# Optimization experiments

Measured on AMD Instinct MI355X. Metric: run time of the kernel, lower is better.

Reference implementation:

```python
import jax, jax.numpy as jnp
import numpy as np

N_NODES = 100000
N_EDGES = 1600000
FACTOR = 0.5
REPEAT = 2


def setup_inputs() -> dict:
    key = jax.random.key(0)
    ks = jax.random.split(key, 8)
    x = jax.random.normal(ks[0], (N_NODES, 32), dtype=jnp.float32)
    edge_val = jax.random.uniform(ks[1], (N_EDGES,), dtype=jnp.float32)
    edge_row = jax.random.randint(ks[2], (N_EDGES,), 0, N_NODES)
    edge_col = jax.random.randint(ks[3], (N_EDGES,), 0, N_NODES)
    W1 = jax.random.normal(ks[4], (32, 64), dtype=jnp.float32) * 0.05
    b1 = jnp.zeros((64,), dtype=jnp.float32)
    W2 = jax.random.normal(ks[5], (64, 64), dtype=jnp.float32) * 0.05
    b2 = jnp.zeros((64,), dtype=jnp.float32)
    return {"x": x, "edge_val": edge_val, "edge_row": edge_row,
            "edge_col": edge_col, "W1": W1, "b1": b1, "W2": W2, "b2": b2}


def _spmm(edge_row, edge_col, edge_val, h):
    # out[r] += (factor * val_e) * h[c]  for each edge e=(r,c)
    gathered = (FACTOR * edge_val)[:, None] * h[edge_col]  # [E, D]
    return jax.ops.segment_sum(gathered, edge_row, num_segments=N_NODES)


def _propagate(edge_row, edge_col, edge_val, h):
    # h = (factor*A)^repeat @ h
    for _ in range(REPEAT):
        h = _spmm(edge_row, edge_col, edge_val, h)
    return h


def reference(x, edge_val, edge_row, edge_col, W1, b1, W2, b2):
    # layer 1: propagate -> linear -> relu
    h = _propagate(edge_row, edge_col, edge_val, x)
    h = jax.nn.relu(h @ W1 + b1)
    # layer 2: propagate -> linear -> identity
    h = _propagate(edge_row, edge_col, edge_val, h)
    h = h @ W2 + b2
    return h
```

## Files before the change

kernel.cpp:

```cpp
#include <hip/hip_runtime.h>
#include <hip/hip_bf16.h>


#define REGION_SHIFT 9
#define REGION_SIZE  (1 << REGION_SHIFT)
#define COL_MASK 0x1FFFF
#define GBUILD 256

typedef unsigned short u16;
typedef unsigned int   u32;
typedef __attribute__((ext_vector_type(8))) short bf16x8;
typedef __attribute__((ext_vector_type(4))) float f32x4;

__device__ inline float bflo(u32 w) { return __uint_as_float(w << 16); }
__device__ inline float bfhi(u32 w) { return __uint_as_float(w & 0xffff0000u); }
__device__ inline u32 bfpack(float a, float b) {
    u32 ua = __float_as_uint(a), ub = __float_as_uint(b);
    ua = (ua + 0x7fffu + ((ua >> 16) & 1u)) >> 16;
    ub = (ub + 0x7fffu + ((ub >> 16) & 1u)) & 0xffff0000u;
    return ua | ub;
}
__device__ inline u16 bf1(float f) {
    u32 u = __float_as_uint(f);
    return (u16)((u + 0x7fffu + ((u >> 16) & 1u)) >> 16);
}

__global__ void region_count_kernel(const int* __restrict__ er, int E,
                                    int* __restrict__ partial,
                                    const float* __restrict__ x,
                                    u16* __restrict__ xb, int n4,
                                    const float* __restrict__ W1,
                                    const float* __restrict__ W2,
                                    u16* __restrict__ W1f,
                                    u16* __restrict__ W2f) {
    for (int i = blockIdx.x * 256 + threadIdx.x; i < n4; i += gridDim.x * 256) {
        float4 a = reinterpret_cast<const float4*>(x)[i];
        uint2 o;
        o.x = bfpack(a.x, a.y);
        o.y = bfpack(a.z, a.w);
        reinterpret_cast<uint2*>(xb)[i] = o;
    }
    if (blockIdx.x == 0) {
        for (int idx = threadIdx.x; idx < 2048; idx += 256) {
            int j = idx & 7, n16 = (idx >> 3) & 15;
            int quad = (idx >> 7) & 3, t = (idx >> 9) & 3;
            W1f[idx] = bf1(W1[(quad * 8 + j) * 64 + t * 16 + n16]);
        }
        for (int idx = threadIdx.x; idx < 4096; idx += 256) {
            int j = idx & 7, n16 = (idx >> 3) & 15;
            int quad = (idx >> 7) & 3, half = (idx >> 9) & 1, t = (idx >> 10) & 3;
            W2f[idx] = bf1(W2[(half * 32 + quad * 8 + j) * 64 + t * 16 + n16]);
        }
    }
    __shared__ int hist[256];
    int t = threadIdx.x;
    hist[t] = 0;
    __syncthreads();
    int chunk = (E + gridDim.x - 1) / gridDim.x;
    int s = blockIdx.x * chunk;
    int e = min(E, s + chunk);
    for (int i = s + t; i < e; i += 256)
        atomicAdd(&hist[er[i] >> REGION_SHIFT], 1);
    __syncthreads();
    partial[blockIdx.x * 256 + t] = hist[t];
}

__global__ void region_scan_kernel(const int* __restrict__ partial,
                                   int* __restrict__ region_off,
                                   int nreg, int E, int G) {
    __shared__ int s[256];
    int t = threadIdx.x;
    int total = 0;
    if (t < nreg)
        for (int b = 0; b < G; b++) total += partial[b * 256 + t];
    s[t] = (t < nreg) ? total : 0;
    __syncthreads();
    for (int off = 1; off < 256; off <<= 1) {
        int x = (t >= off) ? s[t - off] : 0;
        __syncthreads();
        s[t] += x;
        __syncthreads();
    }
    if (t < nreg) region_off[t] = s[t] - total;
    if (t == 0) region_off[nreg] = E;
}

__global__ void region_base_kernel(int* __restrict__ partial,
                                   const int* __restrict__ region_off, int nreg) {
    __shared__ int s[256];
    int r = blockIdx.x;
    if (r >= nreg) return;
    int t = threadIdx.x;
    int c = partial[t * 256 + r];
    s[t] = c;
    __syncthreads();
    for (int off = 1; off < 256; off <<= 1) {
        int x = (t >= off) ? s[t - off] : 0;
        __syncthreads();
        s[t] += x;
        __syncthreads();
    }
    partial[t * 256 + r] = region_off[r] + s[t] - c;
}

__global__ void coarse_scatter_kernel(const int* __restrict__ er,
                                      const int* __restrict__ ec,
                                      const float* __restrict__ ev, int E,
                                      const int* __restrict__ partial,
                                      int2* __restrict__ stg) {
    __shared__ int cnt2[256], gbase[256];
    int t = threadIdx.x;
    cnt2[t] = 0;
    gbase[t] = partial[blockIdx.x * 256 + t];
    __syncthreads();
    int chunk = (E + gridDim.x - 1) / gridDim.x;
    int s0 = blockIdx.x * chunk;
    int e0 = min(E, s0 + chunk);
    for (int i = s0 + t; i < e0; i += 256) {
        int r = er[i];
        int b = r >> REGION_SHIFT;
        int rank = atomicAdd(&cnt2[b], 1);
        int2 rec;
        rec.x = ec[i] | ((r & (REGION_SIZE - 1)) << 17);
        rec.y = (int)bf1(0.5f * ev[i]);
        stg[gbase[b] + rank] = rec;
    }
}

__global__ void region_sort_kernel(const int2* __restrict__ stg,
                                   const int* __restrict__ region_off,
                                   int* __restrict__ row_ptr,
                                   u32* __restrict__ cv, int N, int E) {
    __shared__ int hist[REGION_SIZE];
    __shared__ int wp_local[REGION_SIZE];
    __shared__ int psum[256];
    int cb = blockIdx.x;
    int lo = cb << REGION_SHIFT;
    if (lo >= N) return;
    int hi = min(lo + REGION_SIZE, N);
    int cnt = hi - lo;
    int t = threadIdx.x;
    for (int r = t; r < cnt; r += 256) hist[r] = 0;
    __syncthreads();
    int start = region_off[cb];
    int end   = region_off[cb + 1];
    for (int q = start + t; q < end; q += 256)
        atomicAdd(&hist[stg[q].x >> 17], 1);
    __syncthreads();
    int a0 = (2 * t     < cnt) ? hist[2 * t]     : 0;
    int a1 = (2 * t + 1 < cnt) ? hist[2 * t + 1] : 0;
    psum[t] = a0 + a1;
    __syncthreads();
    for (int off = 1; off < 256; off <<= 1) {
        int x = (t >= off) ? psum[t - off] : 0;
        __syncthreads();
        psum[t] += x;
        __syncthreads();
    }
    int excl = psum[t] - (a0 + a1);
    if (2 * t < cnt) {
        wp_local[2 * t] = start + excl;
        row_ptr[lo + 2 * t] = start + excl;
    }
    if (2 * t + 1 < cnt) {
        wp_local[2 * t + 1] = start + excl + a0;
        row_ptr[lo + 2 * t + 1] = start + excl + a0;
    }
    if (cb == 0 && t == 0) row_ptr[N] = E;
    __syncthreads();
    for (int q = start + t; q < end; q += 256) {
        int2 e = stg[q];
        int lr = e.x >> 17;
        int p = atomicAdd(&wp_local[lr], 1);
        cv[p] = ((u32)e.y << 17) | ((u32)e.x & COL_MASK);
    }
}

__device__ inline void fma8(float acc[8], float v, uint4 w) {
    acc[0] = fmaf(v, bflo(w.x), acc[0]); acc[1] = fmaf(v, bfhi(w.x), acc[1]);
    acc[2] = fmaf(v, bflo(w.y), acc[2]); acc[3] = fmaf(v, bfhi(w.y), acc[3]);
    acc[4] = fmaf(v, bflo(w.z), acc[4]); acc[5] = fmaf(v, bfhi(w.z), acc[5]);
    acc[6] = fmaf(v, bflo(w.w), acc[6]); acc[7] = fmaf(v, bfhi(w.w), acc[7]);
}
__device__ inline float cvval(u32 q) { return __uint_as_float((q >> 17) << 16); }

template <int D>
__device__ inline void spmm_row(const u16* __restrict__ h,
                                const u32* __restrict__ cv,
                                int start, int end, int sub, float acc[8]) {
    int j = start;
    for (; j + 8 <= end; j += 8) {
        u32 q0 = cv[j],     q1 = cv[j + 1], q2 = cv[j + 2], q3 = cv[j + 3];
        u32 q4 = cv[j + 4], q5 = cv[j + 5], q6 = cv[j + 6], q7 = cv[j + 7];
        uint4 w0 = reinterpret_cast<const uint4*>(h + (size_t)(q0 & COL_MASK) * D)[sub];
        uint4 w1 = reinterpret_cast<const uint4*>(h + (size_t)(q1 & COL_MASK) * D)[sub];
        uint4 w2 = reinterpret_cast<const uint4*>(h + (size_t)(q2 & COL_MASK) * D)[sub];
        uint4 w3 = reinterpret_cast<const uint4*>(h + (size_t)(q3 & COL_MASK) * D)[sub];
        uint4 w4 = reinterpret_cast<const uint4*>(h + (size_t)(q4 & COL_MASK) * D)[sub];
        uint4 w5 = reinterpret_cast<const uint4*>(h + (size_t)(q5 & COL_MASK) * D)[sub];
        uint4 w6 = reinterpret_cast<const uint4*>(h + (size_t)(q6 & COL_MASK) * D)[sub];
        uint4 w7 = reinterpret_cast<const uint4*>(h + (size_t)(q7 & COL_MASK) * D)[sub];
        fma8(acc, cvval(q0), w0);
        fma8(acc, cvval(q1), w1);
        fma8(acc, cvval(q2), w2);
        fma8(acc, cvval(q3), w3);
        fma8(acc, cvval(q4), w4);
        fma8(acc, cvval(q5), w5);
        fma8(acc, cvval(q6), w6);
        fma8(acc, cvval(q7), w7);
    }
    for (; j + 4 <= end; j += 4) {
        u32 q0 = cv[j], q1 = cv[j + 1], q2 = cv[j + 2], q3 = cv[j + 3];
        uint4 w0 = reinterpret_cast<const uint4*>(h + (size_t)(q0 & COL_MASK) * D)[sub];
        uint4 w1 = reinterpret_cast<const uint4*>(h + (size_t)(q1 & COL_MASK) * D)[sub];
        uint4 w2 = reinterpret_cast<const uint4*>(h + (size_t)(q2 & COL_MASK) * D)[sub];
        uint4 w3 = reinterpret_cast<const uint4*>(h + (size_t)(q3 & COL_MASK) * D)[sub];
        fma8(acc, cvval(q0), w0);
        fma8(acc, cvval(q1), w1);
        fma8(acc, cvval(q2), w2);
        fma8(acc, cvval(q3), w3);
    }
    for (; j < end; j++) {
        u32 q = cv[j];
        uint4 w = reinterpret_cast<const uint4*>(h + (size_t)(q & COL_MASK) * D)[sub];
        fma8(acc, cvval(q), w);
    }
}

template <int D, bool FINAL>
__global__ __launch_bounds__(256) void spmm_bf16_kernel(
        const u16* __restrict__ h,
        const int* __restrict__ row_ptr,
        const u32* __restrict__ cv,
        void* __restrict__ outp,
        const float* __restrict__ bias,
        int N) {
    constexpr int LPR = D / 8;
    int gid = blockIdx.x * 256 + threadIdx.x;
    int row = gid / LPR;
    int sub = gid % LPR;
    if (row >= N) return;
    int start = row_ptr[row];
    int end   = row_ptr[row + 1];
    float acc[8] = {0.f, 0.f, 0.f, 0.f, 0.f, 0.f, 0.f, 0.f};
    spmm_row<D>(h, cv, start, end, sub, acc);
    if (FINAL) {
        float* op = (float*)outp + (size_t)row * 64 + sub * 8;
#pragma unroll
        for (int k = 0; k < 8; k++) acc[k] += bias[sub * 8 + k];
        reinterpret_cast<float4*>(op)[0] = make_float4(acc[0], acc[1], acc[2], acc[3]);
        reinterpret_cast<float4*>(op)[1] = make_float4(acc[4], acc[5], acc[6], acc[7]);
    } else {
        u16* ob = (u16*)outp + (size_t)row * D + sub * 8;
        uint4 o;
        o.x = bfpack(acc[0], acc[1]);
        o.y = bfpack(acc[2], acc[3]);
        o.z = bfpack(acc[4], acc[5]);
        o.w = bfpack(acc[6], acc[7]);
        reinterpret_cast<uint4*>(ob)[0] = o;
    }
}

__global__ __launch_bounds__(256) void spmm_dense_kernel(
        const u16* __restrict__ h,
        const int* __restrict__ row_ptr,
        const u32* __restrict__ cv,
        const u16* __restrict__ W1f,
        const float* __restrict__ b1,
        const u16* __restrict__ W2f,
        u16* __restrict__ outb,
        int N) {
    __shared__ __align__(16) u16 tiles[4][16][80];
    int tid = threadIdx.x;
    int lane = tid & 63;
    int wave = tid >> 6;
    int tilebase = blockIdx.x * 64 + wave * 16;
    if (tilebase >= N) return;
    int gid = blockIdx.x * 256 + tid;
    int row = gid >> 2;
    int sub = gid & 3;

    bool vr = row < N;
    int start = vr ? row_ptr[row] : 0;
    int end   = vr ? row_ptr[row + 1] : 0;
    float acc[8] = {0.f, 0.f, 0.f, 0.f, 0.f, 0.f, 0.f, 0.f};
    spmm_row<32>(h, cv, start, end, sub, acc);

    u16 (*tile)[80] = tiles[wave];
    {
        uint4 o;
        o.x = bfpack(acc[0], acc[1]);
        o.y = bfpack(acc[2], acc[3]);
        o.z = bfpack(acc[4], acc[5]);
        o.w = bfpack(acc[6], acc[7]);
        *reinterpret_cast<uint4*>(&tile[lane >> 2][sub * 8]) = o;
    }

    int n16 = lane & 15;
    int quad = lane >> 4;
    bf16x8 w1f[4];
    bf16x8 w2f[4][2];
#pragma unroll
    for (int t = 0; t < 4; t++) {
        w1f[t] = *reinterpret_cast<const bf16x8*>(&W1f[((t * 4 + quad) * 16 + n16) * 8]);
        w2f[t][0] = *reinterpret_cast<const bf16x8*>(&W2f[(((t * 2 + 0) * 4 + quad) * 16 + n16) * 8]);
        w2f[t][1] = *reinterpret_cast<const bf16x8*>(&W2f[(((t * 2 + 1) * 4 + quad) * 16 + n16) * 8]);
    }
    float b1v[4];
#pragma unroll
    for (int t = 0; t < 4; t++) b1v[t] = b1[t * 16 + n16];

    bf16x8 a1 = *reinterpret_cast<const bf16x8*>(&tile[n16][quad * 8]);
    f32x4 zero = {0.f, 0.f, 0.f, 0.f};
    f32x4 c[4];
#pragma unroll
    for (int t = 0; t < 4; t++)
        c[t] = __builtin_amdgcn_mfma_f32_16x16x32_bf16(a1, w1f[t], zero, 0, 0, 0);

#pragma unroll
    for (int t = 0; t < 4; t++)
#pragma unroll
        for (int i = 0; i < 4; i++)
            tile[quad * 4 + i][t * 16 + n16] = bf1(fmaxf(c[t][i] + b1v[t], 0.f));

    bf16x8 a2_0 = *reinterpret_cast<const bf16x8*>(&tile[n16][quad * 8]);
    bf16x8 a2_1 = *reinterpret_cast<const bf16x8*>(&tile[n16][32 + quad * 8]);
    f32x4 d[4];
#pragma unroll
    for (int t = 0; t < 4; t++) {
        d[t] = __builtin_amdgcn_mfma_f32_16x16x32_bf16(a2_0, w2f[t][0], zero, 0, 0, 0);
        d[t] = __builtin_amdgcn_mfma_f32_16x16x32_bf16(a2_1, w2f[t][1], d[t], 0, 0, 0);
    }

#pragma unroll
    for (int t = 0; t < 4; t++)
#pragma unroll
        for (int i = 0; i < 4; i++)
            tile[quad * 4 + i][t * 16 + n16] = bf1(d[t][i]);

#pragma unroll
    for (int half = 0; half < 2; half++) {
        int g = half * 512 + lane * 8;
        int r = g >> 6, cc = g & 63;
        int grow = tilebase + r;
        if (grow < N)
            *reinterpret_cast<uint4*>(outb + (size_t)grow * 64 + cc) =
                *reinterpret_cast<const uint4*>(&tile[r][cc]);
    }
}

extern "C" void kernel_launch(void* const* d_in, const int* in_sizes, int n_in,
                              void* d_out, int out_size, void* d_ws, size_t ws_size,
                              hipStream_t stream) {
    const float* x        = (const float*)d_in[0];
    const float* edge_val = (const float*)d_in[1];
    const int*   edge_row = (const int*)d_in[2];
    const int*   edge_col = (const int*)d_in[3];
    const float* W1       = (const float*)d_in[4];
    const float* b1       = (const float*)d_in[5];
    const float* W2       = (const float*)d_in[6];
    const float* b2       = (const float*)d_in[7];
    float* out = (float*)d_out;

    const int N = in_sizes[0] / 32;
    const int E = in_sizes[1];
    const int NREG = (N + REGION_SIZE - 1) >> REGION_SHIFT;

    u16* xb  = (u16*)d_out;
    u16* t0b = xb + (size_t)N * 32;
    u16* t2b = (u16*)d_out + (size_t)N * 64;

    u16*  t3b = (u16*)d_ws;
    int2* stg = (int2*)d_ws;
    int*  row_ptr    = (int*)((char*)d_ws + (size_t)N * 64 * 2);
    int*  region_off = row_ptr + (N + 1);
    int*  partial    = region_off + (NREG + 1);
    size_t wOff = (((size_t)((char*)(partial + GBUILD * 256) - (char*)d_ws)) + 15) & ~(size_t)15;
    u16* W1f = (u16*)((char*)d_ws + wOff);
    u16* W2f = W1f + 2048;
    size_t cvOff = (((size_t)((char*)(W2f + 4096) - (char*)d_ws)) + 15) & ~(size_t)15;
    u32* cv = (u32*)((char*)d_ws + cvOff);

    int n4 = (N * 32) / 4;

    region_count_kernel<<<GBUILD, 256, 0, stream>>>(edge_row, E, partial, x, xb, n4,
                                                    W1, W2, W1f, W2f);
    region_scan_kernel<<<1, 256, 0, stream>>>(partial, region_off, NREG, E, GBUILD);
    region_base_kernel<<<NREG, 256, 0, stream>>>(partial, region_off, NREG);
    coarse_scatter_kernel<<<GBUILD, 256, 0, stream>>>(edge_row, edge_col, edge_val,
                                                      E, partial, stg);
    region_sort_kernel<<<NREG, 256, 0, stream>>>(stg, region_off, row_ptr, cv, N, E);

    int g32 = (N * 4 + 255) / 256;
    int g64 = (N * 8 + 255) / 256;

    spmm_bf16_kernel<32, false><<<g32, 256, 0, stream>>>(xb, row_ptr, cv, t0b, nullptr, N);
    spmm_dense_kernel<<<g32, 256, 0, stream>>>(t0b, row_ptr, cv, W1f, b1, W2f, t2b, N);
    spmm_bf16_kernel<64, false><<<g64, 256, 0, stream>>>(t2b, row_ptr, cv, t3b, nullptr, N);
    spmm_bf16_kernel<64, true><<<g64, 256, 0, stream>>>(t3b, row_ptr, cv, out, b2, N);
}
```

Baseline: 284.2 us.

## Fuse CSR build kernels into one persistent kernel with grid barriers

Merges the five graph-preprocessing kernels (region count, scan, base offsets, coarse scatter, region sort) into a single 256-block kernel that separates the phases with a software grid barrier built on global atomics. This is meant to remove four kernel launch gaps and their tail effects. It adds a memset for the barrier counter. It relies on all 256 blocks being co-resident, and the barrier spin and fences cost time at each phase.

```diff
diff --git a/kernel.cpp b/kernel.cpp
--- a/kernel.cpp
+++ b/kernel.cpp
@@ -5,7 +5,7 @@
 #define REGION_SHIFT 9
 #define REGION_SIZE  (1 << REGION_SHIFT)
 #define COL_MASK 0x1FFFF
-#define GBUILD 256
+#define NBLK 256
 
 typedef unsigned short u16;
 typedef unsigned int   u32;
@@ -25,154 +25,152 @@
     return (u16)((u + 0x7fffu + ((u >> 16) & 1u)) >> 16);
 }
 
-__global__ void region_count_kernel(const int* __restrict__ er, int E,
-                                    int* __restrict__ partial,
-                                    const float* __restrict__ x,
-                                    u16* __restrict__ xb, int n4,
-                                    const float* __restrict__ W1,
-                                    const float* __restrict__ W2,
-                                    u16* __restrict__ W1f,
-                                    u16* __restrict__ W2f) {
-    for (int i = blockIdx.x * 256 + threadIdx.x; i < n4; i += gridDim.x * 256) {
+__device__ inline void gridbar(int* __restrict__ bar) {
+    __syncthreads();
+    if (threadIdx.x == 0) {
+        __threadfence();
+        int g = __hip_atomic_load(&bar[1], __ATOMIC_RELAXED, __HIP_MEMORY_SCOPE_AGENT);
+        int a = __hip_atomic_fetch_add(&bar[0], 1, __ATOMIC_ACQ_REL, __HIP_MEMORY_SCOPE_AGENT);
+        if (a == NBLK - 1) {
+            __hip_atomic_store(&bar[0], 0, __ATOMIC_RELAXED, __HIP_MEMORY_SCOPE_AGENT);
+            __hip_atomic_fetch_add(&bar[1], 1, __ATOMIC_ACQ_REL, __HIP_MEMORY_SCOPE_AGENT);
+        } else {
+            while (__hip_atomic_load(&bar[1], __ATOMIC_ACQUIRE, __HIP_MEMORY_SCOPE_AGENT) == g)
+                __builtin_amdgcn_s_sleep(8);
+        }
+        __threadfence();
+    }
+    __syncthreads();
+}
+
+__global__ __launch_bounds__(256) void build_fused_kernel(
+        const int* __restrict__ er, const int* __restrict__ ec,
+        const float* __restrict__ ev, int E,
+        const float* __restrict__ x, u16* __restrict__ xb, int n4,
+        const float* __restrict__ W1, const float* __restrict__ W2,
+        u16* __restrict__ W1f, u16* __restrict__ W2f,
+        int* __restrict__ partial, int* __restrict__ region_off,
+        int2* __restrict__ stg, int* __restrict__ row_ptr,
+        u32* __restrict__ cv, int N, int nreg, int* __restrict__ bar) {
+    __shared__ int sh_a[REGION_SIZE];
+    __shared__ int sh_b[REGION_SIZE];
+    __shared__ int sh_p[256];
+    int t  = threadIdx.x;
+    int cb = blockIdx.x;
+
+    for (int i = cb * 256 + t; i < n4; i += NBLK * 256) {
         float4 a = reinterpret_cast<const float4*>(x)[i];
         uint2 o;
         o.x = bfpack(a.x, a.y);
         o.y = bfpack(a.z, a.w);
         reinterpret_cast<uint2*>(xb)[i] = o;
     }
-    if (blockIdx.x == 0) {
-        for (int idx = threadIdx.x; idx < 2048; idx += 256) {
+    if (cb == 0) {
+        for (int idx = t; idx < 2048; idx += 256) {
             int j = idx & 7, n16 = (idx >> 3) & 15;
-            int quad = (idx >> 7) & 3, t = (idx >> 9) & 3;
-            W1f[idx] = bf1(W1[(quad * 8 + j) * 64 + t * 16 + n16]);
-        }
-        for (int idx = threadIdx.x; idx < 4096; idx += 256) {
+            int quad = (idx >> 7) & 3, tt = (idx >> 9) & 3;
+            W1f[idx] = bf1(W1[(quad * 8 + j) * 64 + tt * 16 + n16]);
+        }
+        for (int idx = t; idx < 4096; idx += 256) {
             int j = idx & 7, n16 = (idx >> 3) & 15;
-            int quad = (idx >> 7) & 3, half = (idx >> 9) & 1, t = (idx >> 10) & 3;
-            W2f[idx] = bf1(W2[(half * 32 + quad * 8 + j) * 64 + t * 16 + n16]);
-        }
-    }
-    __shared__ int hist[256];
-    int t = threadIdx.x;
-    hist[t] = 0;
-    __syncthreads();
-    int chunk = (E + gridDim.x - 1) / gridDim.x;
-    int s = blockIdx.x * chunk;
-    int e = min(E, s + chunk);
-    for (int i = s + t; i < e; i += 256)
-        atomicAdd(&hist[er[i] >> REGION_SHIFT], 1);
-    __syncthreads();
-    partial[blockIdx.x * 256 + t] = hist[t];
-}
-
-__global__ void region_scan_kernel(const int* __restrict__ partial,
-                                   int* __restrict__ region_off,
-                                   int nreg, int E, int G) {
-    __shared__ int s[256];
-    int t = threadIdx.x;
-    int total = 0;
-    if (t < nreg)
-        for (int b = 0; b < G; b++) total += partial[b * 256 + t];
-    s[t] = (t < nreg) ? total : 0;
-    __syncthreads();
-    for (int off = 1; off < 256; off <<= 1) {
-        int x = (t >= off) ? s[t - off] : 0;
-        __syncthreads();
-        s[t] += x;
-        __syncthreads();
-    }
-    if (t < nreg) region_off[t] = s[t] - total;
-    if (t == 0) region_off[nreg] = E;
-}
-
-__global__ void region_base_kernel(int* __restrict__ partial,
-                                   const int* __restrict__ region_off, int nreg) {
-    __shared__ int s[256];
-    int r = blockIdx.x;
-    if (r >= nreg) return;
-    int t = threadIdx.x;
-    int c = partial[t * 256 + r];
-    s[t] = c;
-    __syncthreads();
-    for (int off = 1; off < 256; off <<= 1) {
-        int x = (t >= off) ? s[t - off] : 0;
-        __syncthreads();
-        s[t] += x;
-        __syncthreads();
-    }
-    partial[t * 256 + r] = region_off[r] + s[t] - c;
-}
-
-__global__ void coarse_scatter_kernel(const int* __restrict__ er,
-                                      const int* __restrict__ ec,
-                                      const float* __restrict__ ev, int E,
-                                      const int* __restrict__ partial,
-                                      int2* __restrict__ stg) {
-    __shared__ int cnt2[256], gbase[256];
-    int t = threadIdx.x;
-    cnt2[t] = 0;
-    gbase[t] = partial[blockIdx.x * 256 + t];
-    __syncthreads();
-    int chunk = (E + gridDim.x - 1) / gridDim.x;
-    int s0 = blockIdx.x * chunk;
+            int quad = (idx >> 7) & 3, half = (idx >> 9) & 1, tt = (idx >> 10) & 3;
+            W2f[idx] = bf1(W2[(half * 32 + quad * 8 + j) * 64 + tt * 16 + n16]);
+        }
+    }
+    sh_a[t] = 0;
+    __syncthreads();
+    int chunk = (E + NBLK - 1) / NBLK;
+    int s0 = cb * chunk;
     int e0 = min(E, s0 + chunk);
+    for (int i = s0 + t; i < e0; i += 256)
+        atomicAdd(&sh_a[er[i] >> REGION_SHIFT], 1);
+    __syncthreads();
+    partial[cb * 256 + t] = sh_a[t];
+    gridbar(bar);
+
+    if (cb == 0) {
+        int total = 0;
+        if (t < nreg)
+            for (int b = 0; b < NBLK; b++) total += partial[b * 256 + t];
+        sh_p[t] = (t < nreg) ? total : 0;
+        __syncthreads();
+        for (int off = 1; off < 256; off <<= 1) {
+            int xv = (t >= off) ? sh_p[t - off] : 0;
+            __syncthreads();
+            sh_p[t] += xv;
+            __syncthreads();
+        }
+        if (t < nreg) region_off[t] = sh_p[t] - total;
+        if (t == 0) region_off[nreg] = E;
+    }
+    gridbar(bar);
+
+    if (cb < nreg) {
+        int c = partial[t * 256 + cb];
+        sh_p[t] = c;
+        __syncthreads();
+        for (int off = 1; off < 256; off <<= 1) {
+            int xv = (t >= off) ? sh_p[t - off] : 0;
+            __syncthreads();
+            sh_p[t] += xv;
+            __syncthreads();
+        }
+        partial[t * 256 + cb] = region_off[cb] + sh_p[t] - c;
+    }
+    gridbar(bar);
+
+    sh_a[t] = 0;
+    sh_b[t] = partial[cb * 256 + t];
+    __syncthreads();
     for (int i = s0 + t; i < e0; i += 256) {
         int r = er[i];
         int b = r >> REGION_SHIFT;
-        int rank = atomicAdd(&cnt2[b], 1);
+        int rank = atomicAdd(&sh_a[b], 1);
         int2 rec;
         rec.x = ec[i] | ((r & (REGION_SIZE - 1)) << 17);
         rec.y = (int)bf1(0.5f * ev[i]);
-        stg[gbase[b] + rank] = rec;
-    }
-}
-
-__global__ void region_sort_kernel(const int2* __restrict__ stg,
-                                   const int* __restrict__ region_off,
-                                   int* __restrict__ row_ptr,
-                                   u32* __restrict__ cv, int N, int E) {
-    __shared__ int hist[REGION_SIZE];
-    __shared__ int wp_local[REGION_SIZE];
-    __shared__ int psum[256];
-    int cb = blockIdx.x;
-    int lo = cb << REGION_SHIFT;
-    if (lo >= N) return;
-    int hi = min(lo + REGION_SIZE, N);
-    int cnt = hi - lo;
-    int t = threadIdx.x;
-    for (int r = t; r < cnt; r += 256) hist[r] = 0;
-    __syncthreads();
-    int start = region_off[cb];
-    int end   = region_off[cb + 1];
-    for (int q = start + t; q < end; q += 256)
-        atomicAdd(&hist[stg[q].x >> 17], 1);
-    __syncthreads();
-    int a0 = (2 * t     < cnt) ? hist[2 * t]     : 0;
-    int a1 = (2 * t + 1 < cnt) ? hist[2 * t + 1] : 0;
-    psum[t] = a0 + a1;
-    __syncthreads();
-    for (int off = 1; off < 256; off <<= 1) {
-        int x = (t >= off) ? psum[t - off] : 0;
-        __syncthreads();
-        psum[t] += x;
-        __syncthreads();
-    }
-    int excl = psum[t] - (a0 + a1);
-    if (2 * t < cnt) {
-        wp_local[2 * t] = start + excl;
-        row_ptr[lo + 2 * t] = start + excl;
-    }
-    if (2 * t + 1 < cnt) {
-        wp_local[2 * t + 1] = start + excl + a0;
-        row_ptr[lo + 2 * t + 1] = start + excl + a0;
-    }
-    if (cb == 0 && t == 0) row_ptr[N] = E;
-    __syncthreads();
-    for (int q = start + t; q < end; q += 256) {
-        int2 e = stg[q];
-        int lr = e.x >> 17;
-        int p = atomicAdd(&wp_local[lr], 1);
-        cv[p] = ((u32)e.y << 17) | ((u32)e.x & COL_MASK);
+        stg[sh_b[b] + rank] = rec;
+    }
+    gridbar(bar);
+
+    if (cb < nreg) {
+        int lo = cb << REGION_SHIFT;
+        int hi = min(lo + REGION_SIZE, N);
+        int cnt = hi - lo;
+        for (int r = t; r < cnt; r += 256) sh_a[r] = 0;
+        __syncthreads();
+        int start = region_off[cb];
+        int end   = region_off[cb + 1];
+        for (int q = start + t; q < end; q += 256)
+            atomicAdd(&sh_a[stg[q].x >> 17], 1);
+        __syncthreads();
+        int a0 = (2 * t     < cnt) ? sh_a[2 * t]     : 0;
+        int a1 = (2 * t + 1 < cnt) ? sh_a[2 * t + 1] : 0;
+        sh_p[t] = a0 + a1;
+        __syncthreads();
+        for (int off = 1; off < 256; off <<= 1) {
+            int xv = (t >= off) ? sh_p[t - off] : 0;
+            __syncthreads();
+            sh_p[t] += xv;
+            __syncthreads();
+        }
+        int excl = sh_p[t] - (a0 + a1);
+        if (2 * t < cnt) {
+            sh_b[2 * t] = start + excl;
+            row_ptr[lo + 2 * t] = start + excl;
+        }
+        if (2 * t + 1 < cnt) {
+            sh_b[2 * t + 1] = start + excl + a0;
+            row_ptr[lo + 2 * t + 1] = start + excl + a0;
+        }
+        if (cb == 0 && t == 0) row_ptr[N] = E;
+        __syncthreads();
+        for (int q = start + t; q < end; q += 256) {
+            int2 e = stg[q];
+            int lr = e.x >> 17;
+            int p = atomicAdd(&sh_b[lr], 1);
+            cv[p] = ((u32)e.y << 17) | ((u32)e.x & COL_MASK);
+        }
     }
 }
 
@@ -375,21 +373,20 @@
     int*  row_ptr    = (int*)((char*)d_ws + (size_t)N * 64 * 2);
     int*  region_off = row_ptr + (N + 1);
     int*  partial    = region_off + (NREG + 1);
-    size_t wOff = (((size_t)((char*)(partial + GBUILD * 256) - (char*)d_ws)) + 15) & ~(size_t)15;
+    size_t wOff = (((size_t)((char*)(partial + NBLK * 256) - (char*)d_ws)) + 15) & ~(size_t)15;
     u16* W1f = (u16*)((char*)d_ws + wOff);
     u16* W2f = W1f + 2048;
     size_t cvOff = (((size_t)((char*)(W2f + 4096) - (char*)d_ws)) + 15) & ~(size_t)15;
     u32* cv = (u32*)((char*)d_ws + cvOff);
+    size_t barOff = (cvOff + (size_t)E * 4 + 255) & ~(size_t)255;
+    int* bar = (int*)((char*)d_ws + barOff);
 
     int n4 = (N * 32) / 4;
 
-    region_count_kernel<<<GBUILD, 256, 0, stream>>>(edge_row, E, partial, x, xb, n4,
-                                                    W1, W2, W1f, W2f);
-    region_scan_kernel<<<1, 256, 0, stream>>>(partial, region_off, NREG, E, GBUILD);
-    region_base_kernel<<<NREG, 256, 0, stream>>>(partial, region_off, NREG);
-    coarse_scatter_kernel<<<GBUILD, 256, 0, stream>>>(edge_row, edge_col, edge_val,
-                                                      E, partial, stg);
-    region_sort_kernel<<<NREG, 256, 0, stream>>>(stg, region_off, row_ptr, cv, N, E);
+    hipMemsetAsync(bar, 0, 16, stream);
+    build_fused_kernel<<<NBLK, 256, 0, stream>>>(
+        edge_row, edge_col, edge_val, E, x, xb, n4,
+        W1, W2, W1f, W2f, partial, region_off, stg, row_ptr, cv, N, NREG, bar);
 
     int g32 = (N * 4 + 255) / 256;
     int g64 = (N * 8 + 255) / 256;
```

After: 450.5 us. 1.59x slower.

## Merge region scan kernels, split staging into key/value arrays, cache region in LDS

Applied to the files above, without the earlier changes.

Fuses the single-block region scan and per-region base kernels into one kernel, where each block recomputes its region offset by reducing the partial counts of earlier regions. The staging buffer changes from int2 records to separate u32 key and u16 value arrays, which cuts staging bytes. The region sort kernel loads each region's edges into LDS once and reuses them for both the histogram and scatter passes, falling back to global memory past the capacity. In exchange it uses much more LDS per block and does redundant prefix work in the scan.

```diff
diff --git a/kernel.cpp b/kernel.cpp
--- a/kernel.cpp
+++ b/kernel.cpp
@@ -6,6 +6,7 @@
 #define REGION_SIZE  (1 << REGION_SHIFT)
 #define COL_MASK 0x1FFFF
 #define GBUILD 256
+#define K4CAP 9216
 
 typedef unsigned short u16;
 typedef unsigned int   u32;
@@ -65,53 +66,51 @@
     partial[blockIdx.x * 256 + t] = hist[t];
 }
 
-__global__ void region_scan_kernel(const int* __restrict__ partial,
-                                   int* __restrict__ region_off,
-                                   int nreg, int E, int G) {
-    __shared__ int s[256];
-    int t = threadIdx.x;
-    int total = 0;
-    if (t < nreg)
-        for (int b = 0; b < G; b++) total += partial[b * 256 + t];
-    s[t] = (t < nreg) ? total : 0;
-    __syncthreads();
-    for (int off = 1; off < 256; off <<= 1) {
-        int x = (t >= off) ? s[t - off] : 0;
-        __syncthreads();
-        s[t] += x;
-        __syncthreads();
-    }
-    if (t < nreg) region_off[t] = s[t] - total;
-    if (t == 0) region_off[nreg] = E;
-}
-
-__global__ void region_base_kernel(int* __restrict__ partial,
-                                   const int* __restrict__ region_off, int nreg) {
+__global__ void region_scanbase_kernel(const int* __restrict__ partial,
+                                       int* __restrict__ bases,
+                                       int* __restrict__ region_off,
+                                       int nreg, int E, int G) {
     __shared__ int s[256];
     int r = blockIdx.x;
     if (r >= nreg) return;
     int t = threadIdx.x;
-    int c = partial[t * 256 + r];
+    int rowsum = 0;
+    const int* prow = partial + t * 256;
+    for (int q = 0; q < r; q++) rowsum += prow[q];
+    s[t] = rowsum;
+    __syncthreads();
+    for (int off = 128; off > 0; off >>= 1) {
+        if (t < off) s[t] += s[t + off];
+        __syncthreads();
+    }
+    int off_r = s[0];
+    __syncthreads();
+    if (t == 0) {
+        region_off[r] = off_r;
+        if (r == 0) region_off[nreg] = E;
+    }
+    int c = prow[r];
     s[t] = c;
     __syncthreads();
     for (int off = 1; off < 256; off <<= 1) {
-        int x = (t >= off) ? s[t - off] : 0;
+        int xv = (t >= off) ? s[t - off] : 0;
         __syncthreads();
-        s[t] += x;
+        s[t] += xv;
         __syncthreads();
     }
-    partial[t * 256 + r] = region_off[r] + s[t] - c;
+    bases[t * 256 + r] = off_r + s[t] - c;
 }
 
 __global__ void coarse_scatter_kernel(const int* __restrict__ er,
                                       const int* __restrict__ ec,
                                       const float* __restrict__ ev, int E,
-                                      const int* __restrict__ partial,
-                                      int2* __restrict__ stg) {
+                                      const int* __restrict__ bases,
+                                      u32* __restrict__ stgk,
+                                      u16* __restrict__ stgv) {
     __shared__ int cnt2[256], gbase[256];
     int t = threadIdx.x;
     cnt2[t] = 0;
-    gbase[t] = partial[blockIdx.x * 256 + t];
+    gbase[t] = bases[blockIdx.x * 256 + t];
     __syncthreads();
     int chunk = (E + gridDim.x - 1) / gridDim.x;
     int s0 = blockIdx.x * chunk;
@@ -120,17 +119,19 @@
         int r = er[i];
         int b = r >> REGION_SHIFT;
         int rank = atomicAdd(&cnt2[b], 1);
-        int2 rec;
-        rec.x = ec[i] | ((r & (REGION_SIZE - 1)) << 17);
-        rec.y = (int)bf1(0.5f * ev[i]);
-        stg[gbase[b] + rank] = rec;
-    }
-}
-
-__global__ void region_sort_kernel(const int2* __restrict__ stg,
+        int p = gbase[b] + rank;
+        stgk[p] = (u32)ec[i] | ((u32)(r & (REGION_SIZE - 1)) << 17);
+        stgv[p] = bf1(0.5f * ev[i]);
+    }
+}
+
+__global__ void region_sort_kernel(const u32* __restrict__ stgk,
+                                   const u16* __restrict__ stgv,
                                    const int* __restrict__ region_off,
                                    int* __restrict__ row_ptr,
                                    u32* __restrict__ cv, int N, int E) {
+    __shared__ u32 sk[K4CAP];
+    __shared__ u16 sv[K4CAP];
     __shared__ int hist[REGION_SIZE];
     __shared__ int wp_local[REGION_SIZE];
     __shared__ int psum[256];
@@ -141,11 +142,18 @@
     int cnt = hi - lo;
     int t = threadIdx.x;
     for (int r = t; r < cnt; r += 256) hist[r] = 0;
-    __syncthreads();
     int start = region_off[cb];
     int end   = region_off[cb + 1];
-    for (int q = start + t; q < end; q += 256)
-        atomicAdd(&hist[stg[q].x >> 17], 1);
+    for (int q = start + t; q < end; q += 256) {
+        int idx = q - start;
+        if (idx < K4CAP) { sk[idx] = stgk[q]; sv[idx] = stgv[q]; }
+    }
+    __syncthreads();
+    for (int q = start + t; q < end; q += 256) {
+        int idx = q - start;
+        u32 key = (idx < K4CAP) ? sk[idx] : stgk[q];
+        atomicAdd(&hist[key >> 17], 1);
+    }
     __syncthreads();
     int a0 = (2 * t     < cnt) ? hist[2 * t]     : 0;
     int a1 = (2 * t + 1 < cnt) ? hist[2 * t + 1] : 0;
@@ -169,10 +177,13 @@
     if (cb == 0 && t == 0) row_ptr[N] = E;
     __syncthreads();
     for (int q = start + t; q < end; q += 256) {
-        int2 e = stg[q];
-        int lr = e.x >> 17;
+        int idx = q - start;
+        u32 key; u32 val;
+        if (idx < K4CAP) { key = sk[idx]; val = sv[idx]; }
+        else             { key = stgk[q]; val = stgv[q]; }
+        int lr = key >> 17;
         int p = atomicAdd(&wp_local[lr], 1);
-        cv[p] = ((u32)e.y << 17) | ((u32)e.x & COL_MASK);
+        cv[p] = (val << 17) | (key & COL_MASK);
     }
 }
 
@@ -370,12 +381,14 @@
     u16* t0b = xb + (size_t)N * 32;
     u16* t2b = (u16*)d_out + (size_t)N * 64;
 
-    u16*  t3b = (u16*)d_ws;
-    int2* stg = (int2*)d_ws;
-    int*  row_ptr    = (int*)((char*)d_ws + (size_t)N * 64 * 2);
-    int*  region_off = row_ptr + (N + 1);
-    int*  partial    = region_off + (NREG + 1);
-    size_t wOff = (((size_t)((char*)(partial + GBUILD * 256) - (char*)d_ws)) + 15) & ~(size_t)15;
+    u16* t3b  = (u16*)d_ws;
+    u32* stgk = (u32*)d_ws;
+    u16* stgv = (u16*)((char*)d_ws + (size_t)E * 4);
+    int* row_ptr    = (int*)((char*)d_ws + (size_t)N * 64 * 2);
+    int* region_off = row_ptr + (N + 1);
+    int* partial    = region_off + (NREG + 1);
+    int* bases      = partial + GBUILD * 256;
+    size_t wOff = (((size_t)((char*)(bases + GBUILD * 256) - (char*)d_ws)) + 15) & ~(size_t)15;
     u16* W1f = (u16*)((char*)d_ws + wOff);
     u16* W2f = W1f + 2048;
     size_t cvOff = (((size_t)((char*)(W2f + 4096) - (char*)d_ws)) + 15) & ~(size_t)15;
@@ -385,11 +398,12 @@
 
     region_count_kernel<<<GBUILD, 256, 0, stream>>>(edge_row, E, partial, x, xb, n4,
                                                     W1, W2, W1f, W2f);
-    region_scan_kernel<<<1, 256, 0, stream>>>(partial, region_off, NREG, E, GBUILD);
-    region_base_kernel<<<NREG, 256, 0, stream>>>(partial, region_off, NREG);
+    region_scanbase_kernel<<<NREG, 256, 0, stream>>>(partial, bases, region_off,
+                                                     NREG, E, GBUILD);
     coarse_scatter_kernel<<<GBUILD, 256, 0, stream>>>(edge_row, edge_col, edge_val,
-                                                      E, partial, stg);
-    region_sort_kernel<<<NREG, 256, 0, stream>>>(stg, region_off, row_ptr, cv, N, E);
+                                                      E, bases, stgk, stgv);
+    region_sort_kernel<<<NREG, 256, 0, stream>>>(stgk, stgv, region_off,
+                                                 row_ptr, cv, N, E);
 
     int g32 = (N * 4 + 255) / 256;
     int g64 = (N * 8 + 255) / 256;
```

After: 282.3 us. No clear change (-0.7%).
